# Kernel tuning notes

Hardware: AMD Instinct MI355X
Metric: run time of the kernel (lower is better)

The kernel has to match this reference:

```python
import jax, jax.numpy as jnp
import numpy as np
import math

HID = 300   # model dim (d_k in the source's scale factor)
HDIM = 64   # attention projection dim
NH = 8      # heads = last axis of view(B,S,HDIM//8,8)
DH = HDIM // NH
L = 6


def pos_encoding(S, d):
    pos = jnp.arange(S, dtype=jnp.float32)[:, None]
    i = jnp.arange(d)
    expo = jnp.where(i % 2 == 0, i, i - 1).astype(jnp.float32) / d
    ang = pos / jnp.power(jnp.float32(10000.0), expo)  # (S, d)
    return jnp.where(i % 2 == 0, jnp.sin(ang), jnp.cos(ang))


def norm(x, g, b):
    mu = jnp.mean(x, axis=-1, keepdims=True)
    var = jnp.var(x, axis=-1, keepdims=True, ddof=1)  # torch.var is unbiased
    return g * (x - mu) / jnp.sqrt(var + 1e-8) + b


def mha(x, mask, wq, wk, wv, wo):
    B, S, _ = x.shape
    # view(B,S,DH,NH).permute(3,0,1,2): head h = feature indices i*NH+h
    q = (x @ wq).reshape(B, S, DH, NH).transpose(3, 0, 1, 2)  # (NH,B,S,DH)
    k = (x @ wk).reshape(B, S, DH, NH).transpose(3, 0, 1, 2)
    v = (x @ wv).reshape(B, S, DH, NH).transpose(3, 0, 1, 2)
    e = jnp.einsum('hbqd,hbkd->hbqk', q, k) / math.sqrt(HID)
    e = jnp.where(mask[None], jnp.float32(-1e9), e)
    alpha = jax.nn.softmax(e, axis=-1)
    h = jnp.einsum('hbqk,hbkd->hbqd', alpha, v)
    # cat(head0..head7, dim=2) -> head-major feature layout
    a = h.transpose(1, 2, 0, 3).reshape(B, S, HDIM)
    return a @ wo


def encoder(x, mask, wq, wk, wv, wo, w1, bb1, w2, bb2, g1, be1, g2, be2):
    x2 = mha(x, mask, wq, wk, wv, wo)
    x = norm(x2 + x, g1, be1)
    ff = jnp.maximum(x @ w1 + bb1, 0.0) @ w2 + bb2
    x = norm(ff + x, g2, be2)
    return x


def setup_inputs() -> dict:
    key = jax.random.key(0)
    ks = jax.random.split(key, 16)
    B, S, V, C = 32, 512, 50000, 1000
    sc = 0.02
    return {
        'x': jax.random.randint(ks[0], (B, S), 0, V),
        'emb': jax.random.normal(ks[1], (V, HID), jnp.float32) * sc,
        'WQ': jax.random.normal(ks[2], (L, HID, HDIM), jnp.float32) * sc,
        'WK': jax.random.normal(ks[3], (L, HID, HDIM), jnp.float32) * sc,
        'WV': jax.random.normal(ks[4], (L, HID, HDIM), jnp.float32) * sc,
        'WO': jax.random.normal(ks[5], (L, HDIM, HID), jnp.float32) * sc,
        'W1': jax.random.normal(ks[6], (L, HID, 4 * HID), jnp.float32) * sc,
        'b1': jax.random.normal(ks[7], (L, 4 * HID), jnp.float32) * sc,
        'W2': jax.random.normal(ks[8], (L, 4 * HID, HID), jnp.float32) * sc,
        'b2': jax.random.normal(ks[9], (L, HID), jnp.float32) * sc,
        'gamma1': jnp.ones((L,), jnp.float32),
        'beta1': jnp.zeros((L,), jnp.float32),
        'gamma2': jnp.ones((L,), jnp.float32),
        'beta2': jnp.zeros((L,), jnp.float32),
        'V_d': jax.random.normal(ks[10], (HID, C), jnp.float32) * sc,
        'gamma_f': jnp.float32(1.0),
        'beta_f': jnp.float32(0.0),
    }


def reference(x, emb, WQ, WK, WV, WO, W1, b1, W2, b2,
              gamma1, beta1, gamma2, beta2, V_d, gamma_f, beta_f):
    B, S = x.shape
    mask = (x == 0)[:, None, :] * jnp.ones((1, S, 1), bool)  # (B,S,S)
    x1 = emb[x]                               # (B,S,HID)
    x2 = x1 + pos_encoding(S, HID)[None]
    acc = x2 + x1                             # dense residual running sum
    out = x2
    for l in range(L):
        out = encoder(acc, mask, WQ[l], WK[l], WV[l], WO[l],
                      W1[l], b1[l], W2[l], b2[l],
                      gamma1[l], beta1[l], gamma2[l], beta2[l])
        acc = acc + out
    logits = jnp.sum(out, axis=1) @ V_d       # (B,C)
    return jax.nn.softmax(norm(logits, gamma_f, beta_f), axis=1)
```

## Files before the change

### kernel.cpp

```cpp
#include <hip/hip_runtime.h>
#include <hip/hip_bf16.h>
#include <cstdio>
#include <cstdint>

#define BATCH 32
#define SEQ 512
#define BSQ (BATCH*SEQ)
#define HIDD 300
#define HD 64
#define NHEAD 8
#define DHEAD 8
#define NLAYERS 6
#define FFD 1200
#define NCLS 1000
#define NSPLIT 4
#define KCH (SEQ/NSPLIT)
#define CLS_KS 4
#define CLS_KC (HIDD/CLS_KS)

typedef short short8 __attribute__((ext_vector_type(8)));
typedef float floatx4 __attribute__((ext_vector_type(4)));

__device__ __forceinline__ short f2b(float v){
  __hip_bfloat16 h = __float2bfloat16(v);
  short s; __builtin_memcpy(&s, &h, 2); return s;
}

__global__ void t10_embed(const int* __restrict__ toks,
                          const float* __restrict__ emb,
                          float* __restrict__ acc,
                          short* __restrict__ accbf){
  int idx = blockIdx.x*256 + threadIdx.x;
  if (idx >= BSQ*320) return;
  int row = idx / 320;
  int j   = idx - row*320;
  if (j >= HIDD){ accbf[(size_t)row*320 + j] = 0; return; }
  int t = toks[row];
  float e = emb[(size_t)t*HIDD + j];
  int s = row & (SEQ-1);
  float expo = (float)(j & ~1) * (1.0f/(float)HIDD);
  float ang  = (float)s * expf(-expo * 9.210340371976184f);
  float pe   = (j & 1) ? cosf(ang) : sinf(ang);
  float v = 2.0f*e + pe;
  acc[(size_t)row*HIDD + j] = v;
  accbf[(size_t)row*320 + j] = f2b(v);
}

__global__ void prep_w(const float* __restrict__ src, short* __restrict__ dst,
                       int K, int N, int Kpad, int rows, int nbase,
                       int sls, int dls, int total, int perm){
  int idx = blockIdx.x*256 + threadIdx.x;
  if (idx >= total) return;
  int l   = idx / (rows*Kpad);
  int rem = idx - l*(rows*Kpad);
  int n = rem / Kpad;
  int k = rem - n*Kpad;
  int sc = perm ? ((n & 7)*8 + (n >> 3)) : n;
  float v = (n < N && k < K) ? src[(size_t)l*sls + (size_t)k*N + sc] : 0.f;
  dst[(size_t)l*dls + (size_t)(nbase+n)*Kpad + k] = f2b(v);
}

__global__ __launch_bounds__(256) void mm_a16(
    const short* __restrict__ A, const short* __restrict__ Wt,
    const float* __restrict__ bias, float* __restrict__ C,
    short* __restrict__ Cb,
    int M, int N, int Kpad, int Npad, int nnb, int relu){
  __shared__ short sA[64][40];
  __shared__ short sB[64][40];
  int wg = blockIdx.x;
  int cpx = gridDim.x >> 3;
  int swz = (wg & 7)*cpx + (wg >> 3);
  int mt = swz / nnb, nt = swz - mt*nnb;
  int m0 = mt*64, n0 = nt*64;
  int tid = threadIdx.x;
  int lane = tid & 63, wv = tid >> 6;
  int wm = (wv & 1)*32, wn = (wv >> 1)*32;
  int l15 = lane & 15, quad = lane >> 4;
  floatx4 acc[2][2] = {};
  int srow = tid >> 2, sko = (tid & 3)*8;
  const short* Arow = A  + (size_t)(m0 + srow)*Kpad + sko;
  const short* Brow = Wt + (size_t)(n0 + srow)*Kpad + sko;
  int nch = Kpad >> 5;
  for (int c = 0; c < nch; c++){
    int k0 = c*32;
    __syncthreads();
    *(short8*)&sA[srow][sko] = *(const short8*)(Arow + k0);
    *(short8*)&sB[srow][sko] = *(const short8*)(Brow + k0);
    __syncthreads();
    short8 af[2], bf[2];
    for (int i=0;i<2;i++)
      af[i] = *(const short8*)&sA[wm + i*16 + l15][quad*8];
    for (int j=0;j<2;j++)
      bf[j] = *(const short8*)&sB[wn + j*16 + l15][quad*8];
    for (int i=0;i<2;i++)
      for (int j=0;j<2;j++)
        acc[i][j] = __builtin_amdgcn_mfma_f32_16x16x32_bf16(af[i], bf[j], acc[i][j], 0,0,0);
  }
  if (Cb){
    for (int j=0;j<2;j++){
      int n = n0 + wn + j*16 + l15;
      float bv = (bias && n < N) ? bias[n] : 0.f;
      for (int i=0;i<2;i++){
        int mbase = m0 + wm + i*16 + quad*4;
        for (int r=0;r<4;r++){
          float cv = acc[i][j][r] + bv;
          if (relu) cv = fmaxf(cv, 0.f);
          Cb[(size_t)(mbase+r)*Npad + n] = (n < N) ? f2b(cv) : (short)0;
        }
      }
    }
  } else {
    for (int j=0;j<2;j++){
      int n = n0 + wn + j*16 + l15;
      if (n >= N) continue;
      float bv = bias ? bias[n] : 0.f;
      for (int i=0;i<2;i++){
        int mbase = m0 + wm + i*16 + quad*4;
        for (int r=0;r<4;r++){
          float cv = acc[i][j][r] + bv;
          if (relu) cv = fmaxf(cv, 0.f);
          C[(size_t)(mbase+r)*N + n] = cv;
        }
      }
    }
  }
}

__global__ __launch_bounds__(256) void t12_attn_part(
    const float* __restrict__ qkv, const int* __restrict__ toks,
    float* __restrict__ pp, float* __restrict__ ps){
  __shared__ float kb[KCH][8];
  __shared__ float vb[KCH][8];
  __shared__ float msk[KCH];
  int blk = blockIdx.x;
  int ks = blk & (NSPLIT-1);
  int bh = blk >> 2;
  int b = bh >> 3, h = bh & 7;
  int tid = threadIdx.x;
  int kbase = ks*KCH;
  {
    int r = tid >> 1, half = (tid & 1)*4;
    const float* src = qkv + (size_t)(b*SEQ + kbase + r)*192 + h*8 + half;
    *(float4*)&kb[r][half] = *(const float4*)(src + 64);
    *(float4*)&vb[r][half] = *(const float4*)(src + 128);
  }
  if (tid < KCH)
    msk[tid] = (toks[b*SEQ + kbase + tid]==0) ? -1e9f : 0.f;
  __syncthreads();
  const float scale = 0.057735026918962574f;
  float q0[8], q1[8];
  {
    const float* s0 = qkv + (size_t)(b*SEQ+tid)*192 + h*8;
    const float* s1 = qkv + (size_t)(b*SEQ+tid+256)*192 + h*8;
    *(float4*)&q0[0] = *(const float4*)s0; *(float4*)&q0[4] = *(const float4*)(s0+4);
    *(float4*)&q1[0] = *(const float4*)s1; *(float4*)&q1[4] = *(const float4*)(s1+4);
  }
  float sum0=0.f, sum1=0.f, o0[8]={}, o1[8]={};
  #pragma unroll 2
  for (int k=0; k<KCH; k++){
    float kr[8], vr[8];
    *(float4*)&kr[0] = *(float4*)&kb[k][0]; *(float4*)&kr[4] = *(float4*)&kb[k][4];
    *(float4*)&vr[0] = *(float4*)&vb[k][0]; *(float4*)&vr[4] = *(float4*)&vb[k][4];
    float s0v=0.f, s1v=0.f;
    for (int d=0; d<8; d++){ s0v = fmaf(q0[d],kr[d],s0v); s1v = fmaf(q1[d],kr[d],s1v); }
    float m = msk[k];
    float p0 = __expf(fminf(fmaf(s0v,scale,m), 60.f));
    float p1 = __expf(fminf(fmaf(s1v,scale,m), 60.f));
    sum0 += p0; sum1 += p1;
    for (int d=0; d<8; d++){ o0[d] = fmaf(p0,vr[d],o0[d]); o1[d] = fmaf(p1,vr[d],o1[d]); }
  }
  size_t sbase = (size_t)ks*BSQ*64;
  float* d0 = pp + sbase + (size_t)(b*SEQ+tid)*64 + h*8;
  float* d1 = pp + sbase + (size_t)(b*SEQ+tid+256)*64 + h*8;
  *(float4*)d0 = *(float4*)&o0[0]; *(float4*)(d0+4) = *(float4*)&o0[4];
  *(float4*)d1 = *(float4*)&o1[0]; *(float4*)(d1+4) = *(float4*)&o1[4];
  size_t pbase = (size_t)ks*BSQ*8;
  ps[pbase + (size_t)(b*SEQ+tid)*8 + h] = sum0;
  ps[pbase + (size_t)(b*SEQ+tid+256)*8 + h] = sum1;
}

__global__ __launch_bounds__(256) void t12_attn_comb(
    const float* __restrict__ pp, const float* __restrict__ ps,
    short* __restrict__ aout){
  int idx = blockIdx.x*256 + threadIdx.x;
  if (idx >= BSQ*8) return;
  float s = 0.f;
  for (int k=0;k<NSPLIT;k++) s += ps[(size_t)k*BSQ*8 + idx];
  float inv = 1.f/s;
  int bsq = idx >> 3, h = idx & 7;
  size_t base = (size_t)bsq*64 + h*8;
  float o[8] = {};
  for (int k=0;k<NSPLIT;k++){
    const float4* p = (const float4*)(pp + (size_t)k*BSQ*64 + base);
    float4 a = p[0], bq = p[1];
    o[0]+=a.x; o[1]+=a.y; o[2]+=a.z; o[3]+=a.w;
    o[4]+=bq.x; o[5]+=bq.y; o[6]+=bq.z; o[7]+=bq.w;
  }
  short8 r;
  for (int d=0;d<8;d++) r[d] = f2b(o[d]*inv);
  *(short8*)(aout + base) = r;
}

__global__ __launch_bounds__(256) void t10_addnorm(
                 const float* __restrict__ xa, const float* __restrict__ xb,
                 float* __restrict__ y, short* __restrict__ ybf,
                 float* __restrict__ accum, short* __restrict__ accbf,
                 const float* __restrict__ gamma, const float* __restrict__ beta,
                 int l){
  __shared__ float red[8];
  int row = blockIdx.x, tid = threadIdx.x;
  size_t base = (size_t)row*HIDD;
  size_t bbase = (size_t)row*320;
  float v0 = xa[base+tid] + xb[base+tid];
  float v1 = 0.f;
  int has1 = (tid+256 < HIDD);
  if (has1) v1 = xa[base+tid+256] + xb[base+tid+256];
  float s = v0+v1, sq = v0*v0+v1*v1;
  for (int off=32; off; off>>=1){ s += __shfl_down(s,off); sq += __shfl_down(sq,off); }
  int lane = tid & 63, w = tid >> 6;
  if (lane==0){ red[w]=s; red[4+w]=sq; }
  __syncthreads();
  float sum = red[0]+red[1]+red[2]+red[3];
  float ssq = red[4]+red[5]+red[6]+red[7];
  float mu  = sum * (1.0f/HIDD);
  float var = (ssq - (float)HIDD*mu*mu) * (1.0f/(HIDD-1));
  float rstd = rsqrtf(var + 1e-8f);
  float g = gamma[l], be = beta[l];
  float o0 = g*(v0-mu)*rstd + be;
  y[base+tid] = o0;
  if (ybf) ybf[bbase+tid] = f2b(o0);
  if (accum){
    float a0 = accum[base+tid] + o0;
    accum[base+tid] = a0;
    if (accbf) accbf[bbase+tid] = f2b(a0);
  }
  if (has1){
    float o1 = g*(v1-mu)*rstd + be;
    y[base+tid+256] = o1;
    if (ybf) ybf[bbase+tid+256] = f2b(o1);
    if (accum){
      float a1 = accum[base+tid+256] + o1;
      accum[base+tid+256] = a1;
      if (accbf) accbf[bbase+tid+256] = f2b(a1);
    }
  } else if (tid+256 < 320){
    if (ybf) ybf[bbase+tid+256] = 0;
    if (accbf) accbf[bbase+tid+256] = 0;
  }
}

__global__ __launch_bounds__(256) void t13_colsum_part(
    const float* __restrict__ outb, float* __restrict__ part){
  int blk = blockIdx.x;
  int b = blk >> 3, c = blk & 7;
  int tid = threadIdx.x;
  size_t base = (size_t)b*SEQ*HIDD + (size_t)c*64*HIDD;
  int j1 = tid + 256;
  float s0 = 0.f, s1 = 0.f;
  for (int t = 0; t < 64; t++){
    const float* row = outb + base + (size_t)t*HIDD;
    s0 += row[tid];
    if (j1 < HIDD) s1 += row[j1];
  }
  float* dst = part + (size_t)(c*BATCH + b)*HIDD;
  dst[tid] = s0;
  if (j1 < HIDD) dst[j1] = s1;
}

__global__ void t13_colsum_comb(const float* __restrict__ part,
                                float* __restrict__ sums){
  int idx = blockIdx.x*256 + threadIdx.x;
  if (idx >= BATCH*HIDD) return;
  float s = 0.f;
  for (int c = 0; c < 8; c++) s += part[(size_t)c*BATCH*HIDD + idx];
  sums[idx] = s;
}

__global__ __launch_bounds__(256) void t13_cls(
    const float* __restrict__ sums, const float* __restrict__ W,
    float* __restrict__ plog){
  int gid = blockIdx.x*256 + threadIdx.x;
  if (gid >= CLS_KS*BATCH*NCLS) return;
  int c = gid / (BATCH*NCLS);
  int rem = gid - c*(BATCH*NCLS);
  int m = rem / NCLS, n = rem - m*NCLS;
  const float* arow = sums + m*HIDD + c*CLS_KC;
  const float* wcol = W + (size_t)c*CLS_KC*NCLS + n;
  float acc = 0.f;
  #pragma unroll 5
  for (int k = 0; k < CLS_KC; k++)
    acc = fmaf(arow[k], wcol[(size_t)k*NCLS], acc);
  plog[gid] = acc;
}

__device__ __forceinline__ float t10_bsum(float val, float* red){
  for (int off=32; off; off>>=1) val += __shfl_down(val, off);
  __syncthreads();
  if ((threadIdx.x & 63)==0) red[threadIdx.x>>6] = val;
  __syncthreads();
  return red[0]+red[1]+red[2]+red[3];
}
__device__ __forceinline__ float t10_bmax(float val, float* red){
  for (int off=32; off; off>>=1) val = fmaxf(val, __shfl_down(val, off));
  __syncthreads();
  if ((threadIdx.x & 63)==0) red[threadIdx.x>>6] = val;
  __syncthreads();
  return fmaxf(fmaxf(red[0],red[1]), fmaxf(red[2],red[3]));
}

__global__ __launch_bounds__(256) void t10_final(
                  const float* __restrict__ plog,
                  const float* __restrict__ gf, const float* __restrict__ bff,
                  float* __restrict__ outp){
  __shared__ float red[4];
  int b = blockIdx.x, tid = threadIdx.x;
  size_t base = (size_t)b*NCLS;
  float v[4];
  float s = 0.f, sq = 0.f;
  for (int t=0;t<4;t++){
    int j = tid + t*256;
    float x = 0.f;
    if (j < NCLS){
      for (int c=0;c<CLS_KS;c++) x += plog[(size_t)c*BATCH*NCLS + base + j];
    }
    v[t] = x; s += x; sq += x*x;
  }
  s  = t10_bsum(s, red);
  sq = t10_bsum(sq, red);
  float mu  = s * (1.0f/NCLS);
  float var = (sq - (float)NCLS*mu*mu) * (1.0f/(NCLS-1));
  float rstd = rsqrtf(var + 1e-8f);
  float g = gf[0], be = bff[0];
  float y[4]; float mx = -1e30f;
  for (int t=0;t<4;t++){
    int j = tid + t*256;
    y[t] = g*(v[t]-mu)*rstd + be;
    if (j < NCLS) mx = fmaxf(mx, y[t]);
  }
  mx = t10_bmax(mx, red);
  float p[4]; float es = 0.f;
  for (int t=0;t<4;t++){
    int j = tid + t*256;
    p[t] = (j < NCLS) ? __expf(y[t]-mx) : 0.f;
    es += p[t];
  }
  es = t10_bsum(es, red);
  float inv = 1.0f/es;
  for (int t=0;t<4;t++){
    int j = tid + t*256;
    if (j < NCLS) outp[base+j] = p[t]*inv;
  }
}

extern "C" void kernel_launch(void* const* d_in, const int* in_sizes, int n_in,
                              void* d_out, int out_size, void* d_ws, size_t ws_size,
                              hipStream_t stream){
  const int*   toks = (const int*)d_in[0];
  const float* emb  = (const float*)d_in[1];
  const float* WQ   = (const float*)d_in[2];
  const float* WK   = (const float*)d_in[3];
  const float* WV   = (const float*)d_in[4];
  const float* WO   = (const float*)d_in[5];
  const float* W1   = (const float*)d_in[6];
  const float* b1   = (const float*)d_in[7];
  const float* W2   = (const float*)d_in[8];
  const float* b2   = (const float*)d_in[9];
  const float* g1   = (const float*)d_in[10];
  const float* be1  = (const float*)d_in[11];
  const float* g2   = (const float*)d_in[12];
  const float* be2  = (const float*)d_in[13];
  const float* Vd   = (const float*)d_in[14];
  const float* gf   = (const float*)d_in[15];
  const float* bff  = (const float*)d_in[16];
  float* outp = (float*)d_out;

  float* acc    = (float*)d_ws;
  float* xn     = acc    + (size_t)BSQ*HIDD;
  float* outb   = xn     + (size_t)BSQ*HIDD;
  float* tmp    = outb   + (size_t)BSQ*HIDD;
  float* qkv    = tmp    + (size_t)BSQ*HIDD;
  float* sums   = qkv    + (size_t)BSQ*192;
  float* logits = sums   + BATCH*HIDD;
  float* pp     = tmp;
  float* ps     = tmp + (size_t)NSPLIT*BSQ*64;
  short* acc_bf = (short*)(logits + BATCH*NCLS);
  short* xn_bf  = acc_bf + (size_t)BSQ*320;
  short* aat_bf = xn_bf  + (size_t)BSQ*320;
  short* ff1_bf = aat_bf + (size_t)BSQ*64;
  short* wqkv = ff1_bf + (size_t)BSQ*1216;
  short* wo   = wqkv + (size_t)6*192*320;
  short* w1t  = wo   + (size_t)6*320*64;
  short* w2t  = w1t  + (size_t)6*1216*320;
  float* cspart = (float*)(w2t + (size_t)6*320*1216);
  float* plog   = cspart + (size_t)8*BATCH*HIDD;

  {
    int tq = 6*64*320;
    prep_w<<<(tq+255)/256,256,0,stream>>>(WQ, wqkv, 300, 64, 320, 64, 0,   19200, 61440, tq, 1);
    prep_w<<<(tq+255)/256,256,0,stream>>>(WK, wqkv, 300, 64, 320, 64, 64,  19200, 61440, tq, 1);
    prep_w<<<(tq+255)/256,256,0,stream>>>(WV, wqkv, 300, 64, 320, 64, 128, 19200, 61440, tq, 1);
    int to = 6*320*64;
    prep_w<<<(to+255)/256,256,0,stream>>>(WO, wo, 64, 300, 64, 320, 0, 19200, 20480, to, 0);
    int t1 = 6*1216*320;
    prep_w<<<(t1+255)/256,256,0,stream>>>(W1, w1t, 300, 1200, 320, 1216, 0, 360000, 389120, t1, 0);
    int t2 = 6*320*1216;
    prep_w<<<(t2+255)/256,256,0,stream>>>(W2, w2t, 1200, 300, 1216, 320, 0, 360000, 389120, t2, 0);
  }

  t10_embed<<<(BSQ*320+255)/256, 256, 0, stream>>>(toks, emb, acc, acc_bf);

  for (int l = 0; l < NLAYERS; l++){
    mm_a16<<<256*3,256,0,stream>>>(acc_bf, wqkv + (size_t)l*61440, nullptr, qkv, nullptr,
                                   BSQ, 192, 320, 0, 3, 0);
    t12_attn_part<<<BATCH*NHEAD*NSPLIT, 256, 0, stream>>>(qkv, toks, pp, ps);
    t12_attn_comb<<<(BSQ*8)/256, 256, 0, stream>>>(pp, ps, aat_bf);
    mm_a16<<<256*5,256,0,stream>>>(aat_bf, wo + (size_t)l*20480, nullptr, tmp, nullptr,
                                   BSQ, 300, 64, 0, 5, 0);
    t10_addnorm<<<BSQ,256,0,stream>>>(tmp, acc, xn, xn_bf, nullptr, nullptr, g1, be1, l);
    mm_a16<<<256*19,256,0,stream>>>(xn_bf, w1t + (size_t)l*389120, b1 + (size_t)l*FFD,
                                    nullptr, ff1_bf, BSQ, 1200, 320, 1216, 19, 1);
    mm_a16<<<256*5,256,0,stream>>>(ff1_bf, w2t + (size_t)l*389120, b2 + (size_t)l*HIDD,
                                   tmp, nullptr, BSQ, 300, 1216, 0, 5, 0);
    t10_addnorm<<<BSQ,256,0,stream>>>(tmp, xn, outb, nullptr, acc, acc_bf, g2, be2, l);
  }

  t13_colsum_part<<<BATCH*8, 256, 0, stream>>>(outb, cspart);
  t13_colsum_comb<<<(BATCH*HIDD+255)/256, 256, 0, stream>>>(cspart, sums);
  t13_cls<<<(CLS_KS*BATCH*NCLS)/256, 256, 0, stream>>>(sums, Vd, plog);
  t10_final<<<BATCH, 256, 0, stream>>>(plog, gf, bff, outp);

  hipStreamCaptureStatus cs = hipStreamCaptureStatusNone;
  hipStreamIsCapturing(stream, &cs);
  if (cs == hipStreamCaptureStatusNone){
    hipError_t e_sync = hipStreamSynchronize(stream);
    float ho[4] = {-1,-1,-1,-1};
    hipMemcpy(ho, d_out, 16, hipMemcpyDeviceToHost);
    fprintf(stderr, "[t13] sync=%s out[0..3]=%g,%g,%g,%g\n",
            hipGetErrorString(e_sync), ho[0], ho[1], ho[2], ho[3]);
    fflush(stderr);
  }
}
```

Measured before the change: 1.230 ms.

## Compute attention partials with bf16 MFMA instead of scalar FMA loops

```diff
diff --git a/kernel.cpp b/kernel.cpp
--- a/kernel.cpp
+++ b/kernel.cpp
@@ -24,6 +24,9 @@
 __device__ __forceinline__ short f2b(float v){
   __hip_bfloat16 h = __float2bfloat16(v);
   short s; __builtin_memcpy(&s, &h, 2); return s;
+}
+__device__ __forceinline__ unsigned pk2(float a, float b){
+  return (unsigned)(unsigned short)f2b(a) | ((unsigned)(unsigned short)f2b(b) << 16);
 }
 
 __global__ void t10_embed(const int* __restrict__ toks,
@@ -126,57 +129,113 @@
   }
 }
 
-__global__ __launch_bounds__(256) void t12_attn_part(
+__global__ __launch_bounds__(256) void t14_attn(
     const float* __restrict__ qkv, const int* __restrict__ toks,
     float* __restrict__ pp, float* __restrict__ ps){
-  __shared__ float kb[KCH][8];
-  __shared__ float vb[KCH][8];
+  __shared__ float kb[KCH][9];
+  __shared__ float vb[KCH][9];
   __shared__ float msk[KCH];
+  __shared__ short Pl[4][16][136];
   int blk = blockIdx.x;
   int ks = blk & (NSPLIT-1);
   int bh = blk >> 2;
   int b = bh >> 3, h = bh & 7;
   int tid = threadIdx.x;
+  int lane = tid & 63, w = tid >> 6;
+  int quad = lane >> 4, l15 = lane & 15;
   int kbase = ks*KCH;
   {
     int r = tid >> 1, half = (tid & 1)*4;
     const float* src = qkv + (size_t)(b*SEQ + kbase + r)*192 + h*8 + half;
-    *(float4*)&kb[r][half] = *(const float4*)(src + 64);
-    *(float4*)&vb[r][half] = *(const float4*)(src + 128);
+    float4 kx = *(const float4*)(src + 64);
+    float4 vx = *(const float4*)(src + 128);
+    kb[r][half+0]=kx.x; kb[r][half+1]=kx.y; kb[r][half+2]=kx.z; kb[r][half+3]=kx.w;
+    vb[r][half+0]=vx.x; vb[r][half+1]=vx.y; vb[r][half+2]=vx.z; vb[r][half+3]=vx.w;
   }
   if (tid < KCH)
     msk[tid] = (toks[b*SEQ + kbase + tid]==0) ? -1e9f : 0.f;
   __syncthreads();
+
+  short8 kfrag[8];
+  #pragma unroll
+  for (int kt=0;kt<8;kt++){
+    short8 f; 
+    #pragma unroll
+    for (int j=0;j<8;j++) f[j] = 0;
+    if (quad == 0){
+      #pragma unroll
+      for (int j=0;j<8;j++) f[j] = f2b(kb[kt*16 + l15][j]);
+    }
+    kfrag[kt] = f;
+  }
+  short8 vfrag[4];
+  #pragma unroll
+  for (int ks2=0;ks2<4;ks2++){
+    short8 f;
+    #pragma unroll
+    for (int j=0;j<8;j++) f[j] = 0;
+    if (l15 < 8){
+      #pragma unroll
+      for (int j=0;j<8;j++) f[j] = f2b(vb[ks2*32 + quad*8 + j][l15]);
+    } else if (l15 == 8){
+      #pragma unroll
+      for (int j=0;j<8;j++) f[j] = (short)0x3F80;
+    }
+    vfrag[ks2] = f;
+  }
   const float scale = 0.057735026918962574f;
-  float q0[8], q1[8];
-  {
-    const float* s0 = qkv + (size_t)(b*SEQ+tid)*192 + h*8;
-    const float* s1 = qkv + (size_t)(b*SEQ+tid+256)*192 + h*8;
-    *(float4*)&q0[0] = *(const float4*)s0; *(float4*)&q0[4] = *(const float4*)(s0+4);
-    *(float4*)&q1[0] = *(const float4*)s1; *(float4*)&q1[4] = *(const float4*)(s1+4);
-  }
-  float sum0=0.f, sum1=0.f, o0[8]={}, o1[8]={};
-  #pragma unroll 2
-  for (int k=0; k<KCH; k++){
-    float kr[8], vr[8];
-    *(float4*)&kr[0] = *(float4*)&kb[k][0]; *(float4*)&kr[4] = *(float4*)&kb[k][4];
-    *(float4*)&vr[0] = *(float4*)&vb[k][0]; *(float4*)&vr[4] = *(float4*)&vb[k][4];
-    float s0v=0.f, s1v=0.f;
-    for (int d=0; d<8; d++){ s0v = fmaf(q0[d],kr[d],s0v); s1v = fmaf(q1[d],kr[d],s1v); }
-    float m = msk[k];
-    float p0 = __expf(fminf(fmaf(s0v,scale,m), 60.f));
-    float p1 = __expf(fminf(fmaf(s1v,scale,m), 60.f));
-    sum0 += p0; sum1 += p1;
-    for (int d=0; d<8; d++){ o0[d] = fmaf(p0,vr[d],o0[d]); o1[d] = fmaf(p1,vr[d],o1[d]); }
-  }
-  size_t sbase = (size_t)ks*BSQ*64;
-  float* d0 = pp + sbase + (size_t)(b*SEQ+tid)*64 + h*8;
-  float* d1 = pp + sbase + (size_t)(b*SEQ+tid+256)*64 + h*8;
-  *(float4*)d0 = *(float4*)&o0[0]; *(float4*)(d0+4) = *(float4*)&o0[4];
-  *(float4*)d1 = *(float4*)&o1[0]; *(float4*)(d1+4) = *(float4*)&o1[4];
-  size_t pbase = (size_t)ks*BSQ*8;
-  ps[pbase + (size_t)(b*SEQ+tid)*8 + h] = sum0;
-  ps[pbase + (size_t)(b*SEQ+tid+256)*8 + h] = sum1;
+
+  for (int t = 0; t < 8; t++){
+    int q0 = w*128 + t*16;
+    short8 qf;
+    #pragma unroll
+    for (int j=0;j<8;j++) qf[j] = 0;
+    if (quad == 0){
+      const float* qsrc = qkv + (size_t)(b*SEQ + q0 + l15)*192 + h*8;
+      float4 a = *(const float4*)qsrc;
+      float4 c = *(const float4*)(qsrc + 4);
+      qf[0]=f2b(a.x*scale); qf[1]=f2b(a.y*scale); qf[2]=f2b(a.z*scale); qf[3]=f2b(a.w*scale);
+      qf[4]=f2b(c.x*scale); qf[5]=f2b(c.y*scale); qf[6]=f2b(c.z*scale); qf[7]=f2b(c.w*scale);
+    }
+    #pragma unroll
+    for (int kt2 = 0; kt2 < 4; kt2++){
+      floatx4 z = {0.f,0.f,0.f,0.f};
+      floatx4 a0 = __builtin_amdgcn_mfma_f32_16x16x32_bf16(kfrag[2*kt2],   qf, z, 0,0,0);
+      floatx4 a1 = __builtin_amdgcn_mfma_f32_16x16x32_bf16(kfrag[2*kt2+1], qf, z, 0,0,0);
+      float p0[4], p1[4];
+      #pragma unroll
+      for (int r=0;r<4;r++){
+        float m0 = msk[(2*kt2)*16   + quad*4 + r];
+        float m1 = msk[(2*kt2+1)*16 + quad*4 + r];
+        p0[r] = __expf(fminf(a0[r] + m0, 60.f));
+        p1[r] = __expf(fminf(a1[r] + m1, 60.f));
+      }
+      uint2 u0, u1;
+      u0.x = pk2(p0[0], p0[1]); u0.y = pk2(p0[2], p0[3]);
+      u1.x = pk2(p1[0], p1[1]); u1.y = pk2(p1[2], p1[3]);
+      *(uint2*)&Pl[w][l15][(2*kt2)*16   + quad*4] = u0;
+      *(uint2*)&Pl[w][l15][(2*kt2+1)*16 + quad*4] = u1;
+    }
+    floatx4 o = {0.f,0.f,0.f,0.f};
+    #pragma unroll
+    for (int ks2=0; ks2<4; ks2++){
+      short8 pa = *(const short8*)&Pl[w][l15][ks2*32 + quad*8];
+      o = __builtin_amdgcn_mfma_f32_16x16x32_bf16(pa, vfrag[ks2], o, 0,0,0);
+    }
+    if (l15 < 8){
+      #pragma unroll
+      for (int r=0;r<4;r++){
+        int q = q0 + quad*4 + r;
+        pp[(size_t)ks*BSQ*64 + (size_t)(b*SEQ+q)*64 + h*8 + l15] = o[r];
+      }
+    } else if (l15 == 8){
+      #pragma unroll
+      for (int r=0;r<4;r++){
+        int q = q0 + quad*4 + r;
+        ps[(size_t)ks*BSQ*8 + (size_t)(b*SEQ+q)*8 + h] = o[r];
+      }
+    }
+  }
 }
 
 __global__ __launch_bounds__(256) void t12_attn_comb(
@@ -412,7 +471,7 @@
   for (int l = 0; l < NLAYERS; l++){
     mm_a16<<<256*3,256,0,stream>>>(acc_bf, wqkv + (size_t)l*61440, nullptr, qkv, nullptr,
                                    BSQ, 192, 320, 0, 3, 0);
-    t12_attn_part<<<BATCH*NHEAD*NSPLIT, 256, 0, stream>>>(qkv, toks, pp, ps);
+    t14_attn<<<BATCH*NHEAD*NSPLIT, 256, 0, stream>>>(qkv, toks, pp, ps);
     t12_attn_comb<<<(BSQ*8)/256, 256, 0, stream>>>(pp, ps, aat_bf);
     mm_a16<<<256*5,256,0,stream>>>(aat_bf, wo + (size_t)l*20480, nullptr, tmp, nullptr,
                                    BSQ, 300, 64, 0, 5, 0);
@@ -435,7 +494,7 @@
     hipError_t e_sync = hipStreamSynchronize(stream);
     float ho[4] = {-1,-1,-1,-1};
     hipMemcpy(ho, d_out, 16, hipMemcpyDeviceToHost);
-    fprintf(stderr, "[t13] sync=%s out[0..3]=%g,%g,%g,%g\n",
+    fprintf(stderr, "[t14] sync=%s out[0..3]=%g,%g,%g,%g\n",
             hipGetErrorString(e_sync), ho[0], ho[1], ho[2], ho[3]);
     fflush(stderr);
   }
```

Measured after the change: 1.127 ms. 1.09x faster.
